# Kernel tuning notes

Hardware: AMD Instinct MI355X
Metric: run time of the kernel (lower is better)

The kernel has to match this reference:

```python
import jax, jax.numpy as jnp
import numpy as np
import math

B, T, D, H = 2, 2048, 1024, 16
DK = D // H


def _alibi_bias(n_heads, seq_len):
    # canonical ALiBi: slope_h = 2^(-8*(h+1)/n_heads), bias[h,i,j] = -slope_h * (i - j) for j<=i
    slopes = jnp.asarray([2.0 ** (-8.0 * (h + 1) / n_heads) for h in range(n_heads)], dtype=jnp.float32)
    pos = jnp.arange(seq_len, dtype=jnp.float32)
    dist = pos[None, :] - pos[:, None]              # [T, T], (j - i)
    return slopes[:, None, None] * dist[None, :, :]  # [H, T, T] (masked out above diagonal anyway)


def setup_inputs() -> dict:
    key = jax.random.key(0)
    ks = jax.random.split(key, 8)
    s = 1.0 / math.sqrt(D)
    return {
        "query": jax.random.normal(ks[0], (B, T, D), dtype=jnp.float32),
        "key": jax.random.normal(ks[1], (B, T, D), dtype=jnp.float32),
        "value": jax.random.normal(ks[2], (B, T, D), dtype=jnp.float32),
        "alibi_bias": _alibi_bias(H, T),
        "Wq": jax.random.normal(ks[3], (D, D), dtype=jnp.float32) * s,
        "Wk": jax.random.normal(ks[4], (D, D), dtype=jnp.float32) * s,
        "Wv": jax.random.normal(ks[5], (D, D), dtype=jnp.float32) * s,
        "Wo": jax.random.normal(ks[6], (D, D), dtype=jnp.float32) * s,
        "bo": jnp.zeros((D,), dtype=jnp.float32),
    }


def reference(query, key, value, alibi_bias, Wq, Wk, Wv, Wo, bo):
    b, tq, d = query.shape
    tk = key.shape[1]
    # projections (torch Linear: x @ W.T)
    Q = (query @ Wq.T).reshape(b, tq, H, DK).transpose(0, 2, 1, 3)  # [B,H,Tq,dk]
    K = (key @ Wk.T).reshape(b, tk, H, DK).transpose(0, 2, 1, 3)
    V = (value @ Wv.T).reshape(b, tk, H, DK).transpose(0, 2, 1, 3)
    scores = jnp.einsum("bhqd,bhkd->bhqk", Q, K) / math.sqrt(DK)   # [B,H,Tq,Tk]
    scores = scores + alibi_bias[None]
    causal = jnp.triu(jnp.ones((tq, tk), dtype=bool), 1)
    scores = jnp.where(causal, jnp.float32(-jnp.inf), scores)
    attn = jax.nn.softmax(scores, axis=-1)
    out = jnp.einsum("bhqk,bhkd->bhqd", attn, V)                   # [B,H,Tq,dk]
    out = out.transpose(0, 2, 1, 3).reshape(b, tq, d)
    return out @ Wo.T + bo
```

## Files before the change

### kernel.cpp

```cpp
#include <hip/hip_runtime.h>
#include <hip/hip_bf16.h>


#define B_  2
#define T_  2048
#define D_  1024
#define H_  16
#define DK_ 64
#define M_  (B_ * T_)

typedef unsigned short u16;
typedef __attribute__((ext_vector_type(8))) short bf16x8;
typedef __attribute__((ext_vector_type(4))) float f32x4;

#define GL16(g, l) __builtin_amdgcn_global_load_lds( \
    (const __attribute__((address_space(1))) unsigned int*)(const void*)(g), \
    (__attribute__((address_space(3))) unsigned int*)(void*)(l), 16, 0, 0)

__device__ __constant__ float d_slopes[16] = {
    0.70710678118654752440f, 0.5f, 0.35355339059327376220f, 0.25f,
    0.17677669529663688110f, 0.125f, 0.088388347648318440550f, 0.0625f,
    0.044194173824159220275f, 0.03125f, 0.022097086912079610137f, 0.015625f,
    0.011048543456039805068f, 0.0078125f, 0.0055242717280199025342f, 0.00390625f};

__device__ __forceinline__ u16 f2bf_bits(float v) {
    union { __hip_bfloat16 h; u16 u; } cv;
    cv.h = __float2bfloat16(v);
    return cv.u;
}

__global__ __launch_bounds__(256) void cvt_all(
    const float* __restrict__ q, const float* __restrict__ k, const float* __restrict__ v,
    const float* __restrict__ wq, const float* __restrict__ wk,
    const float* __restrict__ wv, const float* __restrict__ wo,
    u16* __restrict__ xq, u16* __restrict__ xk, u16* __restrict__ xv,
    u16* __restrict__ uq, u16* __restrict__ uk, u16* __restrict__ uv, u16* __restrict__ uo) {
    const int b = blockIdx.x;
    const float* s; u16* d; int rel;
    if      (b < 2048) { s = q;  d = xq; rel = b; }
    else if (b < 4096) { s = k;  d = xk; rel = b - 2048; }
    else if (b < 6144) { s = v;  d = xv; rel = b - 4096; }
    else if (b < 6656) { s = wq; d = uq; rel = b - 6144; }
    else if (b < 7168) { s = wk; d = uk; rel = b - 6656; }
    else if (b < 7680) { s = wv; d = uv; rel = b - 7168; }
    else               { s = wo; d = uo; rel = b - 7680; }
    const size_t base = (size_t)rel * 2048 + threadIdx.x * 8;
    float4 f0 = *(const float4*)(s + base);
    float4 f1 = *(const float4*)(s + base + 4);
    alignas(16) u16 o[8];
    o[0] = f2bf_bits(f0.x); o[1] = f2bf_bits(f0.y); o[2] = f2bf_bits(f0.z); o[3] = f2bf_bits(f0.w);
    o[4] = f2bf_bits(f1.x); o[5] = f2bf_bits(f1.y); o[6] = f2bf_bits(f1.z); o[7] = f2bf_bits(f1.w);
    *(uint4*)(d + base) = *(const uint4*)o;
}

__global__ __launch_bounds__(256) void gemm_qkv(
    const u16* __restrict__ xq, const u16* __restrict__ xk, const u16* __restrict__ xv,
    const u16* __restrict__ wq, const u16* __restrict__ wk, const u16* __restrict__ wv,
    u16* __restrict__ oq, u16* __restrict__ ok, u16* __restrict__ ov) {
    __shared__ u16 smem[8704];
    u16* As = smem;
    u16* Bs = smem + 4096;

    const int z = blockIdx.z;
    const u16* X = (z == 0) ? xq : (z == 1) ? xk : xv;
    const u16* W = (z == 0) ? wq : (z == 1) ? wk : wv;

    const int tid = threadIdx.x, lane = tid & 63, w = tid >> 6;
    const int l15 = lane & 15, quad = lane >> 4;
    const int wm = w >> 1, wn = w & 1;
    const int m0 = blockIdx.y * 128, n0 = blockIdx.x * 128;
    const int srow = lane >> 2;
    const int skseg = (lane & 3) * 8;

    f32x4 acc[4][4];
#pragma unroll
    for (int mi = 0; mi < 4; ++mi)
#pragma unroll
        for (int ni = 0; ni < 4; ++ni) acc[mi][ni] = f32x4{0.f, 0.f, 0.f, 0.f};

    const u16* ga = X + (size_t)(m0 + w * 32 + srow) * D_ + skseg;
    const u16* gb = W + (size_t)(n0 + w * 32 + srow) * D_ + skseg;
    u16* lA = As + (w * 32) * 32;
    u16* lB = Bs + (w * 32) * 32;

    for (int k0 = 0; k0 < D_; k0 += 32) {
        GL16(ga + k0,             lA);
        GL16(ga + k0 + 16 * D_,   lA + 16 * 32);
        GL16(gb + k0,             lB);
        GL16(gb + k0 + 16 * D_,   lB + 16 * 32);
        __syncthreads();
        bf16x8 af[4], bfr[4];
#pragma unroll
        for (int mi = 0; mi < 4; ++mi)
            af[mi] = *(const bf16x8*)&As[(wm * 64 + mi * 16 + l15) * 32 + quad * 8];
#pragma unroll
        for (int ni = 0; ni < 4; ++ni)
            bfr[ni] = *(const bf16x8*)&Bs[(wn * 64 + ni * 16 + l15) * 32 + quad * 8];
#pragma unroll
        for (int mi = 0; mi < 4; ++mi)
#pragma unroll
            for (int ni = 0; ni < 4; ++ni)
                acc[mi][ni] = __builtin_amdgcn_mfma_f32_16x16x32_bf16(af[mi], bfr[ni], acc[mi][ni], 0, 0, 0);
        __syncthreads();
    }

    if (z < 2) {
        u16* out = (z == 0) ? oq : ok;
#pragma unroll
        for (int mi = 0; mi < 4; ++mi) {
            const int gmb = m0 + wm * 64 + mi * 16 + quad * 4;
#pragma unroll
            for (int ni = 0; ni < 4; ++ni) {
                const int gn = n0 + wn * 64 + ni * 16 + l15;
                const int h = gn >> 6, dk = gn & 63;
#pragma unroll
                for (int r = 0; r < 4; ++r) {
                    const int gm = gmb + r;
                    const int b = gm >> 11, t = gm & (T_ - 1);
                    out[(((size_t)b * H_ + h) * T_ + t) * DK_ + dk] = f2bf_bits(acc[mi][ni][r]);
                }
            }
        }
    } else {
        u16* Cs = smem;
#pragma unroll
        for (int h2 = 0; h2 < 2; ++h2) {
            __syncthreads();
            if (wn == h2) {
#pragma unroll
                for (int mi = 0; mi < 4; ++mi) {
#pragma unroll
                    for (int ni = 0; ni < 4; ++ni) {
                        const int nloc = ni * 16 + l15;
                        const int mloc = wm * 64 + mi * 16 + quad * 4;
                        alignas(8) u16 pk[4];
#pragma unroll
                        for (int r = 0; r < 4; ++r) pk[r] = f2bf_bits(acc[mi][ni][r]);
                        *(uint2*)&Cs[nloc * 136 + mloc] = *(const uint2*)pk;
                    }
                }
            }
            __syncthreads();
            const int nr = tid >> 2;
            const int mseg = (tid & 3) * 32;
            const int gn = n0 + h2 * 64 + nr;
            const int h = gn >> 6, dk = gn & 63;
            const int b = m0 >> 11;
            const int tl = (m0 & (T_ - 1)) + mseg;
            uint4 v0 = *(const uint4*)&Cs[nr * 136 + mseg];
            uint4 v1 = *(const uint4*)&Cs[nr * 136 + mseg + 8];
            uint4 v2 = *(const uint4*)&Cs[nr * 136 + mseg + 16];
            uint4 v3 = *(const uint4*)&Cs[nr * 136 + mseg + 24];
            u16* op = ov + ((size_t)(b * H_ + h) * DK_ + dk) * T_ + tl;
            *(uint4*)op = v0; *(uint4*)(op + 8) = v1;
            *(uint4*)(op + 16) = v2; *(uint4*)(op + 24) = v3;
        }
    }
}

__global__ __launch_bounds__(256) void gemm_out(const u16* __restrict__ X,
                                                const u16* __restrict__ W,
                                                const float* __restrict__ bias,
                                                float* __restrict__ out) {
    __shared__ u16 As[128 * 32];
    __shared__ u16 Bs[64 * 32];

    const int tid = threadIdx.x, lane = tid & 63, w = tid >> 6;
    const int l15 = lane & 15, quad = lane >> 4;
    const int wm = w >> 1, wn = w & 1;
    const int m0 = blockIdx.y * 128, n0 = blockIdx.x * 64;
    const int srow = lane >> 2;
    const int skseg = (lane & 3) * 8;

    f32x4 acc[4][2];
#pragma unroll
    for (int mi = 0; mi < 4; ++mi)
#pragma unroll
        for (int ni = 0; ni < 2; ++ni) acc[mi][ni] = f32x4{0.f, 0.f, 0.f, 0.f};

    const u16* ga = X + (size_t)(m0 + w * 32 + srow) * D_ + skseg;
    const u16* gb = W + (size_t)(n0 + w * 16 + srow) * D_ + skseg;
    u16* lA = As + (w * 32) * 32;
    u16* lB = Bs + (w * 16) * 32;

    for (int k0 = 0; k0 < D_; k0 += 32) {
        GL16(ga + k0,           lA);
        GL16(ga + k0 + 16 * D_, lA + 16 * 32);
        GL16(gb + k0,           lB);
        __syncthreads();
        bf16x8 af[4], bfr[2];
#pragma unroll
        for (int mi = 0; mi < 4; ++mi)
            af[mi] = *(const bf16x8*)&As[(wm * 64 + mi * 16 + l15) * 32 + quad * 8];
#pragma unroll
        for (int ni = 0; ni < 2; ++ni)
            bfr[ni] = *(const bf16x8*)&Bs[(wn * 32 + ni * 16 + l15) * 32 + quad * 8];
#pragma unroll
        for (int mi = 0; mi < 4; ++mi)
#pragma unroll
            for (int ni = 0; ni < 2; ++ni)
                acc[mi][ni] = __builtin_amdgcn_mfma_f32_16x16x32_bf16(af[mi], bfr[ni], acc[mi][ni], 0, 0, 0);
        __syncthreads();
    }

#pragma unroll
    for (int mi = 0; mi < 4; ++mi) {
        const int gmb = m0 + wm * 64 + mi * 16 + quad * 4;
#pragma unroll
        for (int ni = 0; ni < 2; ++ni) {
            const int gn = n0 + wn * 32 + ni * 16 + l15;
            const float bv = bias[gn];
#pragma unroll
            for (int r = 0; r < 4; ++r)
                out[(size_t)(gmb + r) * D_ + gn] = acc[mi][ni][r] + bv;
        }
    }
}

__global__ __launch_bounds__(256, 2) void flash_attn(const u16* __restrict__ Q,
                                                     const u16* __restrict__ K,
                                                     const u16* __restrict__ VT,
                                                     u16* __restrict__ ctx) {
    const int bh = blockIdx.x;
    const int b  = bh >> 4;
    const int h  = bh & 15;
    const int wave = threadIdx.x >> 6;
    const int lane = threadIdx.x & 63;
    const int l15 = lane & 15;
    const int quad = lane >> 4;
    const int qt = gridDim.y - 1 - blockIdx.y;
    const int qb = qt * 64 + wave * 16;
    const float slope = d_slopes[h];

    __shared__ u16 plds[4][16 * 168];
    u16* pl = plds[wave];

    const size_t baseQK = (size_t)bh * T_ * DK_;
    const u16* qptr = Q + baseQK + (size_t)(qb + l15) * DK_ + quad * 8;
    bf16x8 aq0 = *(const bf16x8*)qptr;
    bf16x8 aq1 = *(const bf16x8*)(qptr + 32);

    f32x4 o[4], osum;
#pragma unroll
    for (int t = 0; t < 4; ++t) o[t] = f32x4{0.f, 0.f, 0.f, 0.f};
    osum = f32x4{0.f, 0.f, 0.f, 0.f};

    const f32x4 zero = {0.f, 0.f, 0.f, 0.f};
    bf16x8 ones;
#pragma unroll
    for (int i = 0; i < 8; ++i) ones[i] = (short)0x3F80;

    for (int kb = 0; kb < qb + 16; kb += 128) {
        f32x4 s[8];
#pragma unroll
        for (int t = 0; t < 8; ++t) {
            const u16* kptr = K + baseQK + (size_t)(kb + t * 16 + l15) * DK_ + quad * 8;
            bf16x8 bk0 = *(const bf16x8*)kptr;
            bf16x8 bk1 = *(const bf16x8*)(kptr + 32);
            s[t] = __builtin_amdgcn_mfma_f32_16x16x32_bf16(aq0, bk0, zero, 0, 0, 0);
            s[t] = __builtin_amdgcn_mfma_f32_16x16x32_bf16(aq1, bk1, s[t], 0, 0, 0);
        }

        bf16x8 vf[4][4];
#pragma unroll
        for (int t = 0; t < 4; ++t) {
            const u16* vbase = VT + ((size_t)bh * DK_ + t * 16 + l15) * T_ + kb;
#pragma unroll
            for (int g = 0; g < 4; ++g)
                vf[t][g] = *(const bf16x8*)(vbase + g * 32 + quad * 8);
        }

#pragma unroll
        for (int t = 0; t < 8; ++t) {
#pragma unroll
            for (int r = 0; r < 4; ++r) {
                const int row = qb + quad * 4 + r;
                const int c = kb + t * 16 + l15;
                const float v = s[t][r] * 0.125f + slope * (float)(c - row);
                const float p = (c <= row) ? __expf(v) : 0.f;
                pl[(quad * 4 + r) * 168 + t * 16 + l15] = f2bf_bits(p);
            }
        }

        bf16x8 ap[4];
#pragma unroll
        for (int g = 0; g < 4; ++g)
            ap[g] = *(const bf16x8*)&pl[l15 * 168 + g * 32 + quad * 8];

#pragma unroll
        for (int t = 0; t < 4; ++t)
#pragma unroll
            for (int g = 0; g < 4; ++g)
                o[t] = __builtin_amdgcn_mfma_f32_16x16x32_bf16(ap[g], vf[t][g], o[t], 0, 0, 0);
#pragma unroll
        for (int g = 0; g < 4; ++g)
            osum = __builtin_amdgcn_mfma_f32_16x16x32_bf16(ap[g], ones, osum, 0, 0, 0);
    }

#pragma unroll
    for (int r = 0; r < 4; ++r) {
        const float inv = 1.0f / osum[r];
        const int row = qb + quad * 4 + r;
        u16* cp = ctx + ((size_t)b * T_ + row) * D_ + h * DK_ + l15;
#pragma unroll
        for (int t = 0; t < 4; ++t) cp[t * 16] = f2bf_bits(o[t][r] * inv);
    }
}

extern "C" void kernel_launch(void* const* d_in, const int* in_sizes, int n_in,
                              void* d_out, int out_size, void* d_ws, size_t ws_size,
                              hipStream_t stream) {
    const float* query = (const float*)d_in[0];
    const float* key   = (const float*)d_in[1];
    const float* value = (const float*)d_in[2];
    const float* Wq    = (const float*)d_in[4];
    const float* Wk    = (const float*)d_in[5];
    const float* Wv    = (const float*)d_in[6];
    const float* Wo    = (const float*)d_in[7];
    const float* bo    = (const float*)d_in[8];
    float* out = (float*)d_out;

    const size_t elems  = (size_t)B_ * H_ * T_ * DK_;
    const size_t welems = (size_t)D_ * D_;
    u16* Qb   = (u16*)d_ws;
    u16* Kb   = Qb + elems;
    u16* VTb  = Kb + elems;
    u16* ctxb = VTb + elems;
    u16* Xq   = ctxb + elems;
    u16* Xk   = Xq + elems;
    u16* Xv   = Xk + elems;
    u16* Uq   = Xv + elems;
    u16* Uk   = Uq + welems;
    u16* Uv   = Uk + welems;
    u16* Uo   = Uv + welems;

    dim3 blk(256);
    cvt_all<<<8192, blk, 0, stream>>>(query, key, value, Wq, Wk, Wv, Wo,
                                      Xq, Xk, Xv, Uq, Uk, Uv, Uo);
    gemm_qkv<<<dim3(D_ / 128, M_ / 128, 3), blk, 0, stream>>>(Xq, Xk, Xv, Uq, Uk, Uv, Qb, Kb, VTb);
    flash_attn<<<dim3(B_ * H_, T_ / 64), blk, 0, stream>>>(Qb, Kb, VTb, ctxb);
    gemm_out<<<dim3(D_ / 64, M_ / 128), blk, 0, stream>>>(ctxb, Uo, bo, out);
}
```

Measured before the change: 546.7 us.

## Stage K and V tiles in shared memory cooperatively across waves in flash attention

Each 128-key block of K and V^T is now loaded by all 256 threads with coalesced 16-byte reads into padded LDS buffers, and the four waves read their MFMA operands from LDS. Previously every wave fetched the same K/V fragments straight from global memory. The aim is to cut redundant global/L2 traffic by sharing tiles across waves. The cost is two block-wide barriers per iteration, more LDS use (which may lower occupancy), and no prefetching, so load latency is still exposed.

Result: faster. 506.5 us (-7.4%).

```diff
diff --git a/kernel.cpp b/kernel.cpp
--- a/kernel.cpp
+++ b/kernel.cpp
@@ -224,22 +224,33 @@
     const int bh = blockIdx.x;
     const int b  = bh >> 4;
     const int h  = bh & 15;
-    const int wave = threadIdx.x >> 6;
-    const int lane = threadIdx.x & 63;
+    const int tid = threadIdx.x;
+    const int wave = tid >> 6;
+    const int lane = tid & 63;
     const int l15 = lane & 15;
     const int quad = lane >> 4;
     const int qt = gridDim.y - 1 - blockIdx.y;
     const int qb = qt * 64 + wave * 16;
     const float slope = d_slopes[h];
 
-    __shared__ u16 plds[4][16 * 168];
-    u16* pl = plds[wave];
+    __shared__ u16 Kl[128 * 72];
+    __shared__ u16 Vl[64 * 136];
+    __shared__ u16 Pl[4][16 * 136];
+    u16* pl = Pl[wave];
 
     const size_t baseQK = (size_t)bh * T_ * DK_;
+    const u16* Kg = K + baseQK;
+    const u16* Vg = VT + (size_t)bh * DK_ * T_;
+
     const u16* qptr = Q + baseQK + (size_t)(qb + l15) * DK_ + quad * 8;
     bf16x8 aq0 = *(const bf16x8*)qptr;
     bf16x8 aq1 = *(const bf16x8*)(qptr + 32);
 
+    const int krow = tid >> 3;
+    const int kseg = (tid & 7) * 8;
+    const int vrow = tid >> 4;
+    const int vseg = (tid & 15) * 8;
+
     f32x4 o[4], osum;
 #pragma unroll
     for (int t = 0; t < 4; ++t) o[t] = f32x4{0.f, 0.f, 0.f, 0.f};
@@ -250,51 +261,59 @@
 #pragma unroll
     for (int i = 0; i < 8; ++i) ones[i] = (short)0x3F80;
 
-    for (int kb = 0; kb < qb + 16; kb += 128) {
-        f32x4 s[8];
-#pragma unroll
-        for (int t = 0; t < 8; ++t) {
-            const u16* kptr = K + baseQK + (size_t)(kb + t * 16 + l15) * DK_ + quad * 8;
-            bf16x8 bk0 = *(const bf16x8*)kptr;
-            bf16x8 bk1 = *(const bf16x8*)(kptr + 32);
-            s[t] = __builtin_amdgcn_mfma_f32_16x16x32_bf16(aq0, bk0, zero, 0, 0, 0);
-            s[t] = __builtin_amdgcn_mfma_f32_16x16x32_bf16(aq1, bk1, s[t], 0, 0, 0);
+    const int kend = qt * 64 + 64;
+    for (int kb = 0; kb < kend; kb += 128) {
+        uint4 kreg[4], vreg[4];
+#pragma unroll
+        for (int p = 0; p < 4; ++p)
+            kreg[p] = *(const uint4*)(Kg + (size_t)(kb + p * 32 + krow) * DK_ + kseg);
+#pragma unroll
+        for (int p = 0; p < 4; ++p)
+            vreg[p] = *(const uint4*)(Vg + (size_t)(p * 16 + vrow) * T_ + kb + vseg);
+        __syncthreads();
+#pragma unroll
+        for (int p = 0; p < 4; ++p)
+            *(uint4*)&Kl[(p * 32 + krow) * 72 + kseg] = kreg[p];
+#pragma unroll
+        for (int p = 0; p < 4; ++p)
+            *(uint4*)&Vl[(p * 16 + vrow) * 136 + vseg] = vreg[p];
+        __syncthreads();
+
+        if (kb < qb + 16) {
+            f32x4 s[8];
+#pragma unroll
+            for (int t = 0; t < 8; ++t) {
+                bf16x8 bk0 = *(const bf16x8*)&Kl[(t * 16 + l15) * 72 + quad * 8];
+                bf16x8 bk1 = *(const bf16x8*)&Kl[(t * 16 + l15) * 72 + 32 + quad * 8];
+                s[t] = __builtin_amdgcn_mfma_f32_16x16x32_bf16(aq0, bk0, zero, 0, 0, 0);
+                s[t] = __builtin_amdgcn_mfma_f32_16x16x32_bf16(aq1, bk1, s[t], 0, 0, 0);
+            }
+#pragma unroll
+            for (int t = 0; t < 8; ++t) {
+#pragma unroll
+                for (int r = 0; r < 4; ++r) {
+                    const int row = qb + quad * 4 + r;
+                    const int c = kb + t * 16 + l15;
+                    const float v = s[t][r] * 0.125f + slope * (float)(c - row);
+                    const float p = (c <= row) ? __expf(v) : 0.f;
+                    pl[(quad * 4 + r) * 136 + t * 16 + l15] = f2bf_bits(p);
+                }
+            }
+            bf16x8 ap[4];
+#pragma unroll
+            for (int g = 0; g < 4; ++g)
+                ap[g] = *(const bf16x8*)&pl[l15 * 136 + g * 32 + quad * 8];
+#pragma unroll
+            for (int t = 0; t < 4; ++t)
+#pragma unroll
+                for (int g = 0; g < 4; ++g) {
+                    bf16x8 bv = *(const bf16x8*)&Vl[(t * 16 + l15) * 136 + g * 32 + quad * 8];
+                    o[t] = __builtin_amdgcn_mfma_f32_16x16x32_bf16(ap[g], bv, o[t], 0, 0, 0);
+                }
+#pragma unroll
+            for (int g = 0; g < 4; ++g)
+                osum = __builtin_amdgcn_mfma_f32_16x16x32_bf16(ap[g], ones, osum, 0, 0, 0);
         }
-
-        bf16x8 vf[4][4];
-#pragma unroll
-        for (int t = 0; t < 4; ++t) {
-            const u16* vbase = VT + ((size_t)bh * DK_ + t * 16 + l15) * T_ + kb;
-#pragma unroll
-            for (int g = 0; g < 4; ++g)
-                vf[t][g] = *(const bf16x8*)(vbase + g * 32 + quad * 8);
-        }
-
-#pragma unroll
-        for (int t = 0; t < 8; ++t) {
-#pragma unroll
-            for (int r = 0; r < 4; ++r) {
-                const int row = qb + quad * 4 + r;
-                const int c = kb + t * 16 + l15;
-                const float v = s[t][r] * 0.125f + slope * (float)(c - row);
-                const float p = (c <= row) ? __expf(v) : 0.f;
-                pl[(quad * 4 + r) * 168 + t * 16 + l15] = f2bf_bits(p);
-            }
-        }
-
-        bf16x8 ap[4];
-#pragma unroll
-        for (int g = 0; g < 4; ++g)
-            ap[g] = *(const bf16x8*)&pl[l15 * 168 + g * 32 + quad * 8];
-
-#pragma unroll
-        for (int t = 0; t < 4; ++t)
-#pragma unroll
-            for (int g = 0; g < 4; ++g)
-                o[t] = __builtin_amdgcn_mfma_f32_16x16x32_bf16(ap[g], vf[t][g], o[t], 0, 0, 0);
-#pragma unroll
-        for (int g = 0; g < 4; ++g)
-            osum = __builtin_amdgcn_mfma_f32_16x16x32_bf16(ap[g], ones, osum, 0, 0, 0);
     }
 
 #pragma unroll
```
